# Performance work log

Hardware: AMD Instinct MI355X
Metric: run time of the kernel (lower is better)

The kernel has to match this reference:

```python
import jax, jax.numpy as jnp
import numpy as np

ROPE_BASE = 10000.0

def _rope_tables(seq_len, head_dim, dtype):
    inv_freq = 1.0 / (ROPE_BASE ** (jnp.arange(0, head_dim, 2, dtype=jnp.float32) / head_dim))
    t = jnp.arange(seq_len, dtype=jnp.float32)
    freqs = jnp.einsum('s,d->sd', t, inv_freq)  # [S, D/2]
    return jnp.cos(freqs).astype(dtype), jnp.sin(freqs).astype(dtype)

def _apply_rope(x, cos, sin):
    # x: [B, H, S, D]; cos/sin: [S, D/2]
    half = x.shape[-1] // 2
    x1, x2 = x[..., :half], x[..., half:]
    c = cos[None, None, :, :]
    s = sin[None, None, :, :]
    return jnp.concatenate([x1 * c - x2 * s, x1 * s + x2 * c], axis=-1)

def setup_inputs() -> dict:
    key = jax.random.key(0)
    k1, k2, k3 = jax.random.split(key, 3)
    B, S, dim = 4, 2048, 1024
    x = jax.random.normal(k1, (B, S, dim), dtype=jnp.float32)
    Wqkv = jax.random.normal(k2, (3 * dim, dim), dtype=jnp.float32) * (1.0 / np.sqrt(dim))
    Wout = jax.random.normal(k3, (dim, dim), dtype=jnp.float32) * (1.0 / np.sqrt(dim))
    mask = jnp.tril(jnp.ones((S, S), dtype=bool))[None, None, :, :]  # causal [1,1,S,S]
    return {"x": x, "mask": mask, "Wqkv": Wqkv, "Wout": Wout, "n_heads": 16}

def reference(x, mask, Wqkv, Wout, n_heads):
    B, S, dim = x.shape
    H = n_heads
    D = dim // H
    qkv = jnp.einsum('bsd,ed->bse', x, Wqkv)             # [B,S,3*dim]
    qkv = qkv.reshape(B, S, 3, H, D)
    q = jnp.transpose(qkv[:, :, 0], (0, 2, 1, 3))        # [B,H,S,D]
    k = jnp.transpose(qkv[:, :, 1], (0, 2, 1, 3))
    v = jnp.transpose(qkv[:, :, 2], (0, 2, 1, 3))
    cos, sin = _rope_tables(S, D, x.dtype)
    q = _apply_rope(q, cos, sin)
    k = _apply_rope(k, cos, sin)
    scale = 1.0 / np.sqrt(D).astype(np.float32)
    scores = jnp.einsum('bhsd,bhtd->bhst', q, k) * scale  # [B,H,S,S]
    scores = jnp.where(mask, scores, -jnp.inf)
    attn = jax.nn.softmax(scores, axis=-1)
    out = jnp.einsum('bhst,bhtd->bhsd', attn, v)          # [B,H,S,D]
    out = jnp.transpose(out, (0, 2, 1, 3)).reshape(B, S, dim)
    return jnp.einsum('bsd,ed->bse', out, Wout)
```

## Files before the change

kernel.cpp:

```cpp
#include <hip/hip_runtime.h>
#include <math.h>


typedef __attribute__((ext_vector_type(8))) __bf16 bf16x8;
typedef __attribute__((ext_vector_type(8))) short  short8;
typedef __attribute__((ext_vector_type(4))) short  s16x4;
typedef __attribute__((ext_vector_type(4))) float  f32x4;

#define MFMA16(a, b, c) __builtin_amdgcn_mfma_f32_16x16x32_bf16((a), (b), (c), 0, 0, 0)

static constexpr int    BATCH = 4;
static constexpr int    SEQ   = 2048;
static constexpr int    DIM   = 1024;
static constexpr int    NH    = 16;
static constexpr int    HD    = 64;
static constexpr size_t BHSD  = (size_t)BATCH * NH * SEQ * HD;
static constexpr float  NEGINF = -1e9f;
static constexpr int    PS_LD  = 72;

__device__ __forceinline__ short f2bf(float f) {
    union { float f; unsigned u; } v; v.f = f;
    unsigned r = v.u + 0x7fffu + ((v.u >> 16) & 1u);
    return (short)(r >> 16);
}

__device__ __forceinline__ short8 cvt8(const f32x4 lo, const f32x4 hi) {
    short8 r;
    r[0] = f2bf(lo[0]); r[1] = f2bf(lo[1]); r[2] = f2bf(lo[2]); r[3] = f2bf(lo[3]);
    r[4] = f2bf(hi[0]); r[5] = f2bf(hi[1]); r[6] = f2bf(hi[2]); r[7] = f2bf(hi[3]);
    return r;
}

template <bool F32>
__device__ __forceinline__ short8 ld8(const void* p, size_t row, int K, int k) {
    if constexpr (F32) {
        const float* f = (const float*)p;
        f32x4 lo = *(const f32x4*)&f[row * (size_t)K + k];
        f32x4 hi = *(const f32x4*)&f[row * (size_t)K + k + 4];
        return cvt8(lo, hi);
    } else {
        const short* s = (const short*)p;
        return *(const short8*)&s[row * (size_t)K + k];
    }
}

__device__ __forceinline__ void gload16(const void* g, void* lds) {
    __builtin_amdgcn_global_load_lds(
        (const __attribute__((address_space(1))) void*)g,
        (__attribute__((address_space(3))) void*)lds, 16, 0, 0);
}

__global__ __launch_bounds__(256) void prep_kernel(
    const float* __restrict__ X, const float* __restrict__ Wq,
    const float* __restrict__ Wo, short* __restrict__ Xb,
    short* __restrict__ Wqb, short* __restrict__ Wob,
    float* __restrict__ cosT, float* __restrict__ sinT) {
    const int stride = gridDim.x * blockDim.x;
    for (int idx = blockIdx.x * blockDim.x + threadIdx.x; idx < 3211264; idx += stride) {
        if (idx < 3145728) {
            const float* src; short* dst; int off;
            if (idx < 2097152)      { src = X;  dst = Xb;  off = idx; }
            else if (idx < 2883584) { src = Wq; dst = Wqb; off = idx - 2097152; }
            else                    { src = Wo; dst = Wob; off = idx - 2883584; }
            f32x4 v = *(const f32x4*)&src[(size_t)off * 4];
            s16x4 r;
            r[0] = f2bf(v[0]); r[1] = f2bf(v[1]); r[2] = f2bf(v[2]); r[3] = f2bf(v[3]);
            *(s16x4*)&dst[(size_t)off * 4] = r;
        } else {
            int r = idx - 3145728;
            int s = r >> 5, d = r & 31;
            float ang = (float)s * __expf(-0.28782313662425574f * (float)d);
            float sn, cs;
            sincosf(ang, &sn, &cs);
            cosT[r] = cs; sinT[r] = sn;
        }
    }
}

template <bool AF32, bool BF32>
__device__ __forceinline__ void gemm128_core(
    const void* __restrict__ A, const void* __restrict__ B, int K,
    short* As, short* Bs, int bm, int bn, f32x4 acc[4][4]) {
    const int tid  = threadIdx.x;
    const int lane = tid & 63;
    const int wave = tid >> 6;
    const int quad = lane >> 4;
    const int col  = lane & 15;
    const int wm   = (wave & 1) * 64;
    const int wn   = (wave >> 1) * 64;

    const int r0 = tid >> 2;
    const int r1 = (tid + 256) >> 2;
    const int ko = (tid & 3) * 8;

#pragma unroll
    for (int i = 0; i < 4; ++i)
#pragma unroll
        for (int j = 0; j < 4; ++j) acc[i][j] = f32x4{0.f, 0.f, 0.f, 0.f};

#pragma unroll 1
    for (int k0 = 0; k0 < K; k0 += 32) {
        short8 a0 = ld8<AF32>(A, (size_t)(bm + r0), K, k0 + ko);
        short8 a1 = ld8<AF32>(A, (size_t)(bm + r1), K, k0 + ko);
        short8 b0 = ld8<BF32>(B, (size_t)(bn + r0), K, k0 + ko);
        short8 b1 = ld8<BF32>(B, (size_t)(bn + r1), K, k0 + ko);
        __syncthreads();
        *(short8*)&As[tid * 8]         = a0;
        *(short8*)&As[(tid + 256) * 8] = a1;
        *(short8*)&Bs[tid * 8]         = b0;
        *(short8*)&Bs[(tid + 256) * 8] = b1;
        __syncthreads();

        bf16x8 af[4], bfr[4];
#pragma unroll
        for (int i = 0; i < 4; ++i)
            af[i] = *(const bf16x8*)&As[(wm + i * 16 + col) * 32 + quad * 8];
#pragma unroll
        for (int j = 0; j < 4; ++j)
            bfr[j] = *(const bf16x8*)&Bs[(wn + j * 16 + col) * 32 + quad * 8];
#pragma unroll
        for (int i = 0; i < 4; ++i)
#pragma unroll
            for (int j = 0; j < 4; ++j)
                acc[i][j] = MFMA16(af[i], bfr[j], acc[i][j]);
    }
}

__device__ __forceinline__ void gemm128_lds(
    const short* __restrict__ A, const short* __restrict__ B, int K,
    short* As, short* Bs, int bm, int bn, f32x4 acc[4][4]) {
    const int tid  = threadIdx.x;
    const int lane = tid & 63;
    const int wave = tid >> 6;
    const int quad = lane >> 4;
    const int col  = lane & 15;
    const int wm   = (wave & 1) * 64;
    const int wn   = (wave >> 1) * 64;

    const int r0 = tid >> 2;
    const int r1 = r0 + 64;
    const int ko = (tid & 3) * 8;

    const short* A0 = &A[(size_t)(bm + r0) * K + ko];
    const short* A1 = &A[(size_t)(bm + r1) * K + ko];
    const short* B0 = &B[(size_t)(bn + r0) * K + ko];
    const short* B1 = &B[(size_t)(bn + r1) * K + ko];

    short* As0 = &As[wave * 512];
    short* As1 = &As[2048 + wave * 512];
    short* Bs0 = &Bs[wave * 512];
    short* Bs1 = &Bs[2048 + wave * 512];

#pragma unroll
    for (int i = 0; i < 4; ++i)
#pragma unroll
        for (int j = 0; j < 4; ++j) acc[i][j] = f32x4{0.f, 0.f, 0.f, 0.f};

#pragma unroll 1
    for (int k0 = 0; k0 < K; k0 += 32) {
        __syncthreads();
        gload16(A0 + k0, As0);
        gload16(A1 + k0, As1);
        gload16(B0 + k0, Bs0);
        gload16(B1 + k0, Bs1);
        __syncthreads();

        bf16x8 af[4], bfr[4];
#pragma unroll
        for (int i = 0; i < 4; ++i)
            af[i] = *(const bf16x8*)&As[(wm + i * 16 + col) * 32 + quad * 8];
#pragma unroll
        for (int j = 0; j < 4; ++j)
            bfr[j] = *(const bf16x8*)&Bs[(wn + j * 16 + col) * 32 + quad * 8];
#pragma unroll
        for (int i = 0; i < 4; ++i)
#pragma unroll
            for (int j = 0; j < 4; ++j)
                acc[i][j] = MFMA16(af[i], bfr[j], acc[i][j]);
    }
}

template <bool PRE>
__global__ __launch_bounds__(256, 2) void qkv_rope_kernel(
    const void* __restrict__ X, const void* __restrict__ W,
    const float* __restrict__ cosT, const float* __restrict__ sinT,
    short* __restrict__ Qo, short* __restrict__ Ko, short* __restrict__ VT) {
    __shared__ __align__(16) short As[128 * 32];
    __shared__ __align__(16) short Bs[128 * 32];
    const int bm = blockIdx.y * 128, bn = blockIdx.x * 128;
    const int lane = threadIdx.x & 63, wave = threadIdx.x >> 6;
    const int quad = lane >> 4, col = lane & 15;
    const int wm = (wave & 1) * 64, wn = (wave >> 1) * 64;

    f32x4 acc[4][4];
    if constexpr (PRE)
        gemm128_lds((const short*)X, (const short*)W, 1024, As, Bs, bm, bn, acc);
    else
        gemm128_core<true, true>(X, W, 1024, As, Bs, bm, bn, acc);

    const int n0    = bn + wn;
    const int which = n0 >> 10;
    const int h     = (n0 >> 6) & 15;

    if (which == 2) {
#pragma unroll
        for (int i = 0; i < 4; ++i) {
            int    m = bm + wm + i * 16 + quad * 4;
            int    b = m >> 11, s = m & 2047;
            size_t rowb = (size_t)(b * NH + h) * HD;
#pragma unroll
            for (int j = 0; j < 4; ++j) {
                int   d = j * 16 + col;
                s16x4 pk;
                pk[0] = f2bf(acc[i][j][0]); pk[1] = f2bf(acc[i][j][1]);
                pk[2] = f2bf(acc[i][j][2]); pk[3] = f2bf(acc[i][j][3]);
                *(s16x4*)&VT[(rowb + d) * SEQ + s] = pk;
            }
        }
    } else {
        short* dst = which ? Ko : Qo;
#pragma unroll
        for (int i = 0; i < 4; ++i)
#pragma unroll
            for (int reg = 0; reg < 4; ++reg) {
                int    m = bm + wm + i * 16 + quad * 4 + reg;
                int    b = m >> 11, s = m & 2047;
                size_t base = ((size_t)(b * NH + h) * SEQ + s) * HD;
#pragma unroll
                for (int j = 0; j < 2; ++j) {
                    int   d1 = j * 16 + col;
                    float sn, cs;
                    if constexpr (PRE) {
                        cs = cosT[(s << 5) + d1];
                        sn = sinT[(s << 5) + d1];
                    } else {
                        float inv = __expf(-0.28782313662425574f * (float)d1);
                        sincosf((float)s * inv, &sn, &cs);
                    }
                    float x1 = acc[i][j][reg];
                    float x2 = acc[i][j + 2][reg];
                    dst[base + d1]      = f2bf(x1 * cs - x2 * sn);
                    dst[base + d1 + 32] = f2bf(x1 * sn + x2 * cs);
                }
            }
    }
}

__global__ __launch_bounds__(256, 2) void attn_kernel(
    const short* __restrict__ Q, const short* __restrict__ K,
    const short* __restrict__ VT, short* __restrict__ att) {
    const int b = blockIdx.z, h = blockIdx.y;
    const int tid = threadIdx.x, wave = tid >> 6, lane = tid & 63;
    const int quad = lane >> 4, col = lane & 15;
    const size_t hoff = (size_t)(b * NH + h) * SEQ * HD;
    const short* Qp  = Q + hoff;
    const short* Kp  = K + hoff;
    const short* VTp = VT + hoff;

    __shared__ __align__(16) short Kt[64 * 64];
    __shared__ __align__(16) short Vt[64 * 64];
    __shared__ __align__(16) short Ps[4 * 32 * PS_LD];

    const int r0 = tid >> 3;
    const int r1 = r0 + 32;
    const int c8 = (tid & 7) * 8;
    const int cs = c8 ^ ((r0 & 7) << 3);
    const int swc = (col & 7) << 3;
    const int cA  = (quad * 8) ^ swc;
    const int cB  = (32 + quad * 8) ^ swc;
    short* Pw = &Ps[wave * 32 * PS_LD];

#pragma unroll 1
    for (int pass = 0; pass < 2; ++pass) {
        const int qt   = pass ? 15 - (int)blockIdx.x : (int)blockIdx.x;
        const int q0   = qt * 128 + wave * 32;
        const int tmax = 2 * qt + 1;

        bf16x8 aq[2][2];
#pragma unroll
        for (int s2 = 0; s2 < 2; ++s2) {
            aq[s2][0] = *(const bf16x8*)&Qp[(q0 + s2 * 16 + col) * HD + quad * 8];
            aq[s2][1] = *(const bf16x8*)&Qp[(q0 + s2 * 16 + col) * HD + 32 + quad * 8];
        }

        float m_i[2][4], l_i[2][4];
        f32x4 o[2][4];
#pragma unroll
        for (int s2 = 0; s2 < 2; ++s2)
#pragma unroll
            for (int rr = 0; rr < 4; ++rr) {
                m_i[s2][rr] = NEGINF; l_i[s2][rr] = 0.f;
                o[s2][rr] = f32x4{0.f, 0.f, 0.f, 0.f};
            }

        short8 ka = *(const short8*)&Kp[r0 * HD + c8];
        short8 kb = *(const short8*)&Kp[r1 * HD + c8];
        short8 va = *(const short8*)&VTp[(size_t)r0 * SEQ + c8];
        short8 vb = *(const short8*)&VTp[(size_t)r1 * SEQ + c8];

#pragma unroll 1
        for (int t = 0; t <= tmax; ++t) {
            const int kt = t * 64;
            __syncthreads();
            *(short8*)&Kt[r0 * 64 + cs] = ka;
            *(short8*)&Kt[r1 * 64 + cs] = kb;
            *(short8*)&Vt[r0 * 64 + cs] = va;
            *(short8*)&Vt[r1 * 64 + cs] = vb;
            __syncthreads();

            if (t < tmax) {
                const int kn = kt + 64;
                ka = *(const short8*)&Kp[(kn + r0) * HD + c8];
                kb = *(const short8*)&Kp[(kn + r1) * HD + c8];
                va = *(const short8*)&VTp[(size_t)r0 * SEQ + kn + c8];
                vb = *(const short8*)&VTp[(size_t)r1 * SEQ + kn + c8];
            }

            if (kt > q0 + 31) continue;

            float p[2][4][4];
            __builtin_amdgcn_s_setprio(1);
#pragma unroll
            for (int jn = 0; jn < 4; ++jn) {
                bf16x8 b0 = *(const bf16x8*)&Kt[(jn * 16 + col) * 64 + cA];
                bf16x8 b1 = *(const bf16x8*)&Kt[(jn * 16 + col) * 64 + cB];
#pragma unroll
                for (int s2 = 0; s2 < 2; ++s2) {
                    f32x4 s = f32x4{0.f, 0.f, 0.f, 0.f};
                    s = MFMA16(aq[s2][0], b0, s);
                    s = MFMA16(aq[s2][1], b1, s);
                    if (t >= 2 * qt) {
#pragma unroll
                        for (int reg = 0; reg < 4; ++reg) {
                            int qr = q0 + s2 * 16 + quad * 4 + reg;
                            int kc = kt + jn * 16 + col;
                            p[s2][jn][reg] = (kc <= qr) ? s[reg] * 0.125f : NEGINF;
                        }
                    } else {
#pragma unroll
                        for (int reg = 0; reg < 4; ++reg)
                            p[s2][jn][reg] = s[reg] * 0.125f;
                    }
                }
            }
            __builtin_amdgcn_s_setprio(0);

#pragma unroll
            for (int s2 = 0; s2 < 2; ++s2) {
                float lm[4];
#pragma unroll
                for (int reg = 0; reg < 4; ++reg)
                    lm[reg] = fmaxf(fmaxf(p[s2][0][reg], p[s2][1][reg]),
                                    fmaxf(p[s2][2][reg], p[s2][3][reg]));
                int ok = (lm[0] <= m_i[s2][0] + 8.f) & (lm[1] <= m_i[s2][1] + 8.f) &
                         (lm[2] <= m_i[s2][2] + 8.f) & (lm[3] <= m_i[s2][3] + 8.f);
                if (__all(ok)) {
#pragma unroll
                    for (int reg = 0; reg < 4; ++reg) {
                        float rs = 0.f;
#pragma unroll
                        for (int jn = 0; jn < 4; ++jn) {
                            p[s2][jn][reg] = __expf(p[s2][jn][reg] - m_i[s2][reg]);
                            rs += p[s2][jn][reg];
                        }
                        l_i[s2][reg] += rs;
                    }
                } else {
                    float alpha[4];
#pragma unroll
                    for (int reg = 0; reg < 4; ++reg) {
                        float mx = lm[reg];
#pragma unroll
                        for (int off = 8; off >= 1; off >>= 1)
                            mx = fmaxf(mx, __shfl_xor(mx, off, 64));
                        float mn   = fmaxf(m_i[s2][reg], mx);
                        alpha[reg] = __expf(m_i[s2][reg] - mn);
                        float rs = 0.f;
#pragma unroll
                        for (int jn = 0; jn < 4; ++jn) {
                            p[s2][jn][reg] = __expf(p[s2][jn][reg] - mn);
                            rs += p[s2][jn][reg];
                        }
                        l_i[s2][reg] = l_i[s2][reg] * alpha[reg] + rs;
                        m_i[s2][reg] = mn;
                    }
#pragma unroll
                    for (int jd = 0; jd < 4; ++jd)
#pragma unroll
                        for (int reg = 0; reg < 4; ++reg)
                            o[s2][jd][reg] *= alpha[reg];
                }

#pragma unroll
                for (int jn = 0; jn < 4; ++jn)
#pragma unroll
                    for (int reg = 0; reg < 4; ++reg)
                        Pw[(s2 * 16 + quad * 4 + reg) * PS_LD + jn * 16 + col] =
                            f2bf(p[s2][jn][reg]);
            }

            bf16x8 ap[2][2];
#pragma unroll
            for (int s2 = 0; s2 < 2; ++s2) {
                ap[s2][0] = *(const bf16x8*)&Pw[(s2 * 16 + col) * PS_LD + quad * 8];
                ap[s2][1] = *(const bf16x8*)&Pw[(s2 * 16 + col) * PS_LD + 32 + quad * 8];
            }
            __builtin_amdgcn_s_setprio(1);
#pragma unroll
            for (int jd = 0; jd < 4; ++jd) {
                bf16x8 bv0 = *(const bf16x8*)&Vt[(jd * 16 + col) * 64 + cA];
                bf16x8 bv1 = *(const bf16x8*)&Vt[(jd * 16 + col) * 64 + cB];
#pragma unroll
                for (int s2 = 0; s2 < 2; ++s2) {
                    o[s2][jd] = MFMA16(ap[s2][0], bv0, o[s2][jd]);
                    o[s2][jd] = MFMA16(ap[s2][1], bv1, o[s2][jd]);
                }
            }
            __builtin_amdgcn_s_setprio(0);
        }

#pragma unroll
        for (int s2 = 0; s2 < 2; ++s2) {
#pragma unroll
            for (int off = 8; off >= 1; off >>= 1)
#pragma unroll
                for (int reg = 0; reg < 4; ++reg)
                    l_i[s2][reg] += __shfl_xor(l_i[s2][reg], off, 64);
            float inv_l[4];
#pragma unroll
            for (int reg = 0; reg < 4; ++reg) inv_l[reg] = 1.f / l_i[s2][reg];
#pragma unroll
            for (int jd = 0; jd < 4; ++jd)
#pragma unroll
                for (int reg = 0; reg < 4; ++reg) {
                    int s = q0 + s2 * 16 + quad * 4 + reg;
                    att[((size_t)(b * SEQ + s)) * DIM + h * HD + jd * 16 + col] =
                        f2bf(o[s2][jd][reg] * inv_l[reg]);
                }
        }
    }
}

template <bool PRE>
__global__ __launch_bounds__(256, 2) void out_gemm_kernel(
    const short* __restrict__ A, const void* __restrict__ W,
    float* __restrict__ out) {
    __shared__ __align__(16) short As[128 * 32];
    __shared__ __align__(16) short Bs[128 * 32];
    const int bm = blockIdx.y * 128, bn = blockIdx.x * 128;
    const int lane = threadIdx.x & 63, wave = threadIdx.x >> 6;
    const int quad = lane >> 4, col = lane & 15;
    const int wm = (wave & 1) * 64, wn = (wave >> 1) * 64;

    f32x4 acc[4][4];
    if constexpr (PRE)
        gemm128_lds(A, (const short*)W, 1024, As, Bs, bm, bn, acc);
    else
        gemm128_core<false, true>(A, W, 1024, As, Bs, bm, bn, acc);

#pragma unroll
    for (int i = 0; i < 4; ++i)
#pragma unroll
        for (int reg = 0; reg < 4; ++reg) {
            int    m    = bm + wm + i * 16 + quad * 4 + reg;
            size_t base = (size_t)m * DIM + bn + wn;
#pragma unroll
            for (int j = 0; j < 4; ++j)
                out[base + j * 16 + col] = acc[i][j][reg];
        }
}

extern "C" void kernel_launch(void* const* d_in, const int* in_sizes, int n_in,
                              void* d_out, int out_size, void* d_ws, size_t ws_size,
                              hipStream_t stream) {
    const float* x    = nullptr;
    const float* Wqkv = nullptr;
    const float* Wout = nullptr;
    for (int i = 0; i < n_in; ++i) {
        switch (in_sizes[i]) {
            case 8388608: x    = (const float*)d_in[i]; break;
            case 3145728: Wqkv = (const float*)d_in[i]; break;
            case 1048576: Wout = (const float*)d_in[i]; break;
            default: break;
        }
    }
    if (!x || !Wqkv || !Wout) return;

    short* Q  = (short*)d_ws;
    short* K  = Q + BHSD;
    short* VT = K + BHSD;
    float* out = (float*)d_out;

    const size_t need_pre = (size_t)4 * BHSD * sizeof(short)
                          + BHSD * sizeof(short)
                          + (size_t)3145728 * sizeof(short)
                          + (size_t)1048576 * sizeof(short)
                          + (size_t)2 * 65536 * sizeof(float);

    if (ws_size >= need_pre) {
        short* att  = VT + BHSD;
        short* Xb   = att + BHSD;
        short* Wqb  = Xb + BHSD;
        short* Wob  = Wqb + 3145728;
        float* cosT = (float*)(Wob + 1048576);
        float* sinT = cosT + 65536;

        prep_kernel<<<dim3(2048), 256, 0, stream>>>(x, Wqkv, Wout, Xb, Wqb, Wob, cosT, sinT);
        qkv_rope_kernel<true><<<dim3(24, 64), 256, 0, stream>>>(Xb, Wqb, cosT, sinT, Q, K, VT);
        attn_kernel<<<dim3(8, NH, BATCH), 256, 0, stream>>>(Q, K, VT, att);
        out_gemm_kernel<true><<<dim3(8, 64), 256, 0, stream>>>(att, Wob, out);
    } else {
        qkv_rope_kernel<false><<<dim3(24, 64), 256, 0, stream>>>(
            x, Wqkv, nullptr, nullptr, Q, K, VT);

        const bool direct = ws_size >= (size_t)4 * BHSD * sizeof(short);
        short* att_dst = direct ? (VT + BHSD) : (short*)d_out;
        attn_kernel<<<dim3(8, NH, BATCH), 256, 0, stream>>>(Q, K, VT, att_dst);

        short* att = att_dst;
        if (!direct) {
            att = (short*)d_ws;
            hipMemcpyAsync(att, att_dst, BHSD * sizeof(short), hipMemcpyDeviceToDevice, stream);
        }
        out_gemm_kernel<false><<<dim3(8, 64), 256, 0, stream>>>(att, Wout, out);
    }
}
```

Measured before the change: 287.5 us.

## Double-buffer GEMM LDS tiles with BK=64 and XOR-swizzled layout

Replaces the single-buffered direct-to-LDS GEMM loop with a two-stage pipeline. Each 64-wide K tile is prefetched two iterations ahead, and vmcnt waits replace the double __syncthreads. The LDS layout is XOR-swizzled to avoid bank conflicts on the fragment reads, and K-step doubles to 64, which halves the barrier count. This raises LDS use to 64KB per block in the QKV and output GEMM kernels, which may limit occupancy with the declared two blocks per CU.

```diff
diff --git a/kernel.cpp b/kernel.cpp
--- a/kernel.cpp
+++ b/kernel.cpp
@@ -126,7 +126,7 @@
     }
 }
 
-__device__ __forceinline__ void gemm128_lds(
+__device__ __forceinline__ void gemm128_p2(
     const short* __restrict__ A, const short* __restrict__ B, int K,
     short* As, short* Bs, int bm, int bn, f32x4 acc[4][4]) {
     const int tid  = threadIdx.x;
@@ -137,47 +137,70 @@
     const int wm   = (wave & 1) * 64;
     const int wn   = (wave >> 1) * 64;
 
-    const int r0 = tid >> 2;
-    const int r1 = r0 + 64;
-    const int ko = (tid & 3) * 8;
-
-    const short* A0 = &A[(size_t)(bm + r0) * K + ko];
-    const short* A1 = &A[(size_t)(bm + r1) * K + ko];
-    const short* B0 = &B[(size_t)(bn + r0) * K + ko];
-    const short* B1 = &B[(size_t)(bn + r1) * K + ko];
-
-    short* As0 = &As[wave * 512];
-    short* As1 = &As[2048 + wave * 512];
-    short* Bs0 = &Bs[wave * 512];
-    short* Bs1 = &Bs[2048 + wave * 512];
+    const int nt = K >> 6;
+    const int rr = tid >> 3;
+    const int swk = (((tid & 7) ^ (rr & 7)) << 3);
+    const short* Ab = &A[(size_t)(bm + rr) * K + swk];
+    const short* Bb = &B[(size_t)(bn + rr) * K + swk];
 
 #pragma unroll
     for (int i = 0; i < 4; ++i)
 #pragma unroll
         for (int j = 0; j < 4; ++j) acc[i][j] = f32x4{0.f, 0.f, 0.f, 0.f};
 
+#define STAGE_TILE(c)                                                         \
+    {                                                                         \
+        const int s_ = (c) & 1;                                               \
+        const int k0_ = (c) << 6;                                             \
+        _Pragma("unroll")                                                     \
+        for (int q = 0; q < 4; ++q) {                                         \
+            gload16(Ab + (size_t)(q * 32) * K + k0_,                          \
+                    &As[s_ * 8192 + q * 2048 + wave * 512]);                  \
+            gload16(Bb + (size_t)(q * 32) * K + k0_,                          \
+                    &Bs[s_ * 8192 + q * 2048 + wave * 512]);                  \
+        }                                                                     \
+    }
+
+    STAGE_TILE(0);
+    STAGE_TILE(1);
+
+    const int pc0 = ((quad) ^ (col & 7)) << 3;
+    const int pc1 = ((4 | quad) ^ (col & 7)) << 3;
+
 #pragma unroll 1
-    for (int k0 = 0; k0 < K; k0 += 32) {
-        __syncthreads();
-        gload16(A0 + k0, As0);
-        gload16(A1 + k0, As1);
-        gload16(B0 + k0, Bs0);
-        gload16(B1 + k0, Bs1);
-        __syncthreads();
-
-        bf16x8 af[4], bfr[4];
-#pragma unroll
-        for (int i = 0; i < 4; ++i)
-            af[i] = *(const bf16x8*)&As[(wm + i * 16 + col) * 32 + quad * 8];
-#pragma unroll
-        for (int j = 0; j < 4; ++j)
-            bfr[j] = *(const bf16x8*)&Bs[(wn + j * 16 + col) * 32 + quad * 8];
-#pragma unroll
-        for (int i = 0; i < 4; ++i)
-#pragma unroll
-            for (int j = 0; j < 4; ++j)
-                acc[i][j] = MFMA16(af[i], bfr[j], acc[i][j]);
-    }
+    for (int c = 0; c < nt; ++c) {
+        const int s = c & 1;
+        if (c + 1 < nt) { asm volatile("s_waitcnt vmcnt(8)" ::: "memory"); }
+        else            { asm volatile("s_waitcnt vmcnt(0)" ::: "memory"); }
+        __builtin_amdgcn_s_barrier();
+
+        const short* Asl = &As[s * 8192];
+        const short* Bsl = &Bs[s * 8192];
+        bf16x8 af[4][2], bfr[4][2];
+#pragma unroll
+        for (int i = 0; i < 4; ++i) {
+            const int r = (wm + i * 16 + col) * 64;
+            af[i][0] = *(const bf16x8*)&Asl[r + pc0];
+            af[i][1] = *(const bf16x8*)&Asl[r + pc1];
+        }
+#pragma unroll
+        for (int j = 0; j < 4; ++j) {
+            const int r = (wn + j * 16 + col) * 64;
+            bfr[j][0] = *(const bf16x8*)&Bsl[r + pc0];
+            bfr[j][1] = *(const bf16x8*)&Bsl[r + pc1];
+        }
+#pragma unroll
+        for (int kk = 0; kk < 2; ++kk)
+#pragma unroll
+            for (int i = 0; i < 4; ++i)
+#pragma unroll
+                for (int j = 0; j < 4; ++j)
+                    acc[i][j] = MFMA16(af[i][kk], bfr[j][kk], acc[i][j]);
+
+        __builtin_amdgcn_s_barrier();
+        if (c + 2 < nt) STAGE_TILE(c + 2);
+    }
+#undef STAGE_TILE
 }
 
 template <bool PRE>
@@ -185,8 +208,8 @@
     const void* __restrict__ X, const void* __restrict__ W,
     const float* __restrict__ cosT, const float* __restrict__ sinT,
     short* __restrict__ Qo, short* __restrict__ Ko, short* __restrict__ VT) {
-    __shared__ __align__(16) short As[128 * 32];
-    __shared__ __align__(16) short Bs[128 * 32];
+    __shared__ __align__(16) short As[2 * 8192];
+    __shared__ __align__(16) short Bs[2 * 8192];
     const int bm = blockIdx.y * 128, bn = blockIdx.x * 128;
     const int lane = threadIdx.x & 63, wave = threadIdx.x >> 6;
     const int quad = lane >> 4, col = lane & 15;
@@ -194,7 +217,7 @@
 
     f32x4 acc[4][4];
     if constexpr (PRE)
-        gemm128_lds((const short*)X, (const short*)W, 1024, As, Bs, bm, bn, acc);
+        gemm128_p2((const short*)X, (const short*)W, 1024, As, Bs, bm, bn, acc);
     else
         gemm128_core<true, true>(X, W, 1024, As, Bs, bm, bn, acc);
 
@@ -445,8 +468,8 @@
 __global__ __launch_bounds__(256, 2) void out_gemm_kernel(
     const short* __restrict__ A, const void* __restrict__ W,
     float* __restrict__ out) {
-    __shared__ __align__(16) short As[128 * 32];
-    __shared__ __align__(16) short Bs[128 * 32];
+    __shared__ __align__(16) short As[2 * 8192];
+    __shared__ __align__(16) short Bs[2 * 8192];
     const int bm = blockIdx.y * 128, bn = blockIdx.x * 128;
     const int lane = threadIdx.x & 63, wave = threadIdx.x >> 6;
     const int quad = lane >> 4, col = lane & 15;
@@ -454,7 +477,7 @@
 
     f32x4 acc[4][4];
     if constexpr (PRE)
-        gemm128_lds(A, (const short*)W, 1024, As, Bs, bm, bn, acc);
+        gemm128_p2(A, (const short*)W, 1024, As, Bs, bm, bn, acc);
     else
         gemm128_core<false, true>(A, W, 1024, As, Bs, bm, bn, acc);
 
```

Result: faster. 278.1 us (-3.2%).
